# Optimization experiments

Hardware: AMD Instinct MI355X
Metric: run time of the kernel (lower is better)

Reference implementation:

```python
import jax, jax.numpy as jnp
import numpy as np

B, N, D, H = 32, 64, 128, 256
LN_EPS = 1e-5


def _mlp(x, W1, b1, g, beta, W2, b2):
    # Linear -> LayerNorm -> GELU (exact erf) -> Linear
    h = x @ W1 + b1
    mu = jnp.mean(h, axis=-1, keepdims=True)
    var = jnp.var(h, axis=-1, keepdims=True)
    h = (h - mu) * jax.lax.rsqrt(var + LN_EPS) * g + beta
    h = jax.nn.gelu(h, approximate=False)
    return h @ W2 + b2


def setup_inputs() -> dict:
    key = jax.random.key(0)
    ks = jax.random.split(key, 10)
    s = lambda fan_in: 1.0 / np.sqrt(fan_in)
    return {
        "slots": jax.random.normal(ks[0], (B, N, D), dtype=jnp.float32),
        "adjacency": jax.random.uniform(ks[1], (B, N, N), dtype=jnp.float32),
        # edge_net params
        "We1": jax.random.uniform(ks[2], (2 * D, H), minval=-s(2 * D), maxval=s(2 * D), dtype=jnp.float32),
        "be1": jnp.zeros((H,), jnp.float32),
        "ge": jnp.ones((H,), jnp.float32),
        "bge": jnp.zeros((H,), jnp.float32),
        "We2": jax.random.uniform(ks[3], (H, D), minval=-s(H), maxval=s(H), dtype=jnp.float32),
        "be2": jnp.zeros((D,), jnp.float32),
        # node_net params
        "Wn1": jax.random.uniform(ks[4], (2 * D, H), minval=-s(2 * D), maxval=s(2 * D), dtype=jnp.float32),
        "bn1": jnp.zeros((H,), jnp.float32),
        "gn": jnp.ones((H,), jnp.float32),
        "bgn": jnp.zeros((H,), jnp.float32),
        "Wn2": jax.random.uniform(ks[5], (H, D), minval=-s(H), maxval=s(H), dtype=jnp.float32),
        "bn2": jnp.zeros((D,), jnp.float32),
    }


def reference(slots, adjacency, We1, be1, ge, bge, We2, be2, Wn1, bn1, gn, bgn, Wn2, bn2):
    b, n, d = slots.shape
    # all-pairs edge features: receiver i, sender j -> [B,N,N,2D]
    ei = jnp.broadcast_to(slots[:, :, None, :], (b, n, n, d))
    ej = jnp.broadcast_to(slots[:, None, :, :], (b, n, n, d))
    edge_feat = jnp.concatenate([ei, ej], axis=-1)
    edge_out = _mlp(edge_feat, We1, be1, ge, bge, We2, be2)  # [B,N,N,D]
    # mask diagonal (i != j) and weight by adjacency, then reduce over j
    mask = 1.0 - jnp.eye(n, dtype=slots.dtype)
    w = adjacency * mask  # [B,N,N]
    messages = jnp.einsum('bij,bijd->bid', w, edge_out)
    node_input = jnp.concatenate([slots, messages], axis=-1)
    delta = _mlp(node_input, Wn1, bn1, gn, bgn, Wn2, bn2)
    return slots + delta
```

## Files before the change

### kernel.cpp

```cpp
#include <hip/hip_runtime.h>

#define NB 32
#define NN 64
#define ND 128
#define NH 256
#define LN_EPS 1e-5f
#define IBLK 4
#define RP 4

__device__ __forceinline__ float gelu_fast(float x) {
    const float z  = fabsf(x) * 0.70710678118654752440f;
    const float t  = __builtin_amdgcn_rcpf(fmaf(0.3275911f, z, 1.0f));
    float p = fmaf(1.061405429f, t, -1.453152027f);
    p = fmaf(p, t, 1.421413741f);
    p = fmaf(p, t, -0.284496736f);
    p = fmaf(p, t, 0.254829592f);
    p = p * t;
    const float e  = __expf(-z * z);
    const float er = copysignf(fmaf(-p, e, 1.0f), x);
    const float sx = 0.5f * x;
    return fmaf(sx, er, sx);
}

__global__ __launch_bounds__(256) void k_pq(const float* __restrict__ slots,
                                            const float* __restrict__ We1,
                                            const float* __restrict__ be1,
                                            float* __restrict__ Pt,
                                            float* __restrict__ Qm) {
    const int r0 = blockIdx.x * RP;
    const int t  = threadIdx.x;
    float pt[RP], qq[RP];
    const float bb = be1[t];
    #pragma unroll
    for (int r = 0; r < RP; ++r) { pt[r] = bb; qq[r] = 0.f; }
    const float* w1 = We1 + t;
    #pragma unroll 2
    for (int dc = 0; dc < ND / 4; ++dc) {
        float xs[RP][4];
        #pragma unroll
        for (int r = 0; r < RP; ++r) {
            const float4 x4 = ((const float4*)(slots + (size_t)(r0 + r) * ND))[dc];
            xs[r][0] = x4.x; xs[r][1] = x4.y; xs[r][2] = x4.z; xs[r][3] = x4.w;
        }
        #pragma unroll
        for (int i = 0; i < 4; ++i) {
            const int d = dc * 4 + i;
            const float wt  = w1[d * NH];
            const float wbt = w1[(ND + d) * NH];
            #pragma unroll
            for (int r = 0; r < RP; ++r) {
                pt[r] = fmaf(xs[r][i], wt,  pt[r]);
                qq[r] = fmaf(xs[r][i], wbt, qq[r]);
            }
        }
    }
    #pragma unroll
    for (int r = 0; r < RP; ++r) {
        Pt[(size_t)(r0 + r) * NH + t] = pt[r];
        Qm[(size_t)(r0 + r) * NH + t] = qq[r];
    }
}

__global__ __launch_bounds__(256) void k_fused(
    const float* __restrict__ slots,
    const float* __restrict__ adj,
    const float* __restrict__ Pt,
    const float* __restrict__ Qm,
    const float* __restrict__ ge,  const float* __restrict__ bge,
    const float* __restrict__ We2, const float* __restrict__ be2,
    const float* __restrict__ Wn1, const float* __restrict__ bn1,
    const float* __restrict__ gn,  const float* __restrict__ bgn,
    const float* __restrict__ Wn2, const float* __restrict__ bn2,
    float* __restrict__ out)
{
    __shared__ float  lds_pt[IBLK][NH];
    __shared__ float  lds_x [IBLK][ND];
    __shared__ float4 lds_wmr[IBLK][NN];
    __shared__ float  lds_s [4][IBLK][NH];
    __shared__ float  lds_sf[IBLK][NH];
    __shared__ float  lds_nin[IBLK][2 * ND];
    __shared__ float  lds_g [IBLK][NH];
    __shared__ float  lds_redA[4][IBLK], lds_redB[4][IBLK];
    __shared__ float  lds_wsum[IBLK];
    __shared__ float  lds_mu[IBLK], lds_rr[IBLK];

    const int blk  = blockIdx.x;
    const int b    = blk >> 4;
    const int i0   = (blk & 15) * IBLK;
    const int r0   = b * NN + i0;
    const int t    = threadIdx.x;
    const int lane = t & 63;
    const int wave = t >> 6;
    const int c    = t & 127;
    const int rg   = t >> 7;

    #pragma unroll
    for (int r = 0; r < IBLK; ++r)
        lds_pt[r][t] = Pt[(size_t)(r0 + r) * NH + t];
    lds_x[rg][c]     = slots[(size_t)(r0 + rg) * ND + c];
    lds_x[rg + 2][c] = slots[(size_t)(r0 + rg + 2) * ND + c];
    {
        float av = adj[(size_t)(r0 + wave) * NN + lane];
        if (lane == i0 + wave) av = 0.f;
        lds_wmr[wave][lane].x = av;
        float ws = av;
        #pragma unroll
        for (int off = 32; off; off >>= 1) ws += __shfl_xor(ws, off);
        if (lane == 0) lds_wsum[wave] = ws;
    }
    __syncthreads();

    {
        float a[IBLK], bq[IBLK];
        #pragma unroll
        for (int r = 0; r < IBLK; ++r) { const float p = lds_pt[r][t]; a[r] = p; bq[r] = p * p; }
        #pragma unroll
        for (int off = 32; off; off >>= 1) {
            #pragma unroll
            for (int r = 0; r < IBLK; ++r) {
                a[r]  += __shfl_xor(a[r],  off);
                bq[r] += __shfl_xor(bq[r], off);
            }
        }
        if (lane == 0) {
            #pragma unroll
            for (int r = 0; r < IBLK; ++r) { lds_redA[wave][r] = a[r]; lds_redB[wave][r] = bq[r]; }
        }
    }
    const int jp   = t >> 2;
    const int part = t & 3;
    float cd[IBLK] = {0.f, 0.f, 0.f, 0.f};
    float qs = 0.f, qs2 = 0.f;
    {
        const float4* qrow = (const float4*)(Qm + ((size_t)b * NN + jp) * NH) + part * 16;
        #pragma unroll 4
        for (int k = 0; k < 16; ++k) {
            const int kk = (k + part * 4) & 15;
            const float4 q = qrow[kk];
            qs  += (q.x + q.y) + (q.z + q.w);
            qs2  = fmaf(q.x, q.x, fmaf(q.y, q.y, fmaf(q.z, q.z, fmaf(q.w, q.w, qs2))));
            #pragma unroll
            for (int r = 0; r < IBLK; ++r) {
                const float4 p = ((const float4*)lds_pt[r])[part * 16 + kk];
                cd[r] = fmaf(p.x, q.x, fmaf(p.y, q.y, fmaf(p.z, q.z, fmaf(p.w, q.w, cd[r]))));
            }
        }
        #pragma unroll
        for (int off = 1; off < 4; off <<= 1) {
            qs += __shfl_xor(qs, off); qs2 += __shfl_xor(qs2, off);
            #pragma unroll
            for (int r = 0; r < IBLK; ++r) cd[r] += __shfl_xor(cd[r], off);
        }
    }
    __syncthreads();
    if (part == 0) {
        const float inv = 1.0f / NH;
        #pragma unroll
        for (int r = 0; r < IBLK; ++r) {
            const float SP1 = (lds_redA[0][r] + lds_redA[1][r]) + (lds_redA[2][r] + lds_redA[3][r]);
            const float SP2 = (lds_redB[0][r] + lds_redB[1][r]) + (lds_redB[2][r] + lds_redB[3][r]);
            const float mu  = (SP1 + qs) * inv;
            const float e2  = (SP2 + 2.f * cd[r] + qs2) * inv;
            lds_wmr[r][jp].y = mu;
            lds_wmr[r][jp].z = __builtin_amdgcn_rsqf(e2 - mu * mu + LN_EPS);
        }
    }
    __syncthreads();

    float4 P[IBLK], A[IBLK];
    #pragma unroll
    for (int r = 0; r < IBLK; ++r) {
        P[r] = ((const float4*)lds_pt[r])[lane];
        A[r] = make_float4(0.f, 0.f, 0.f, 0.f);
    }
    const float4 G  = ((const float4*)ge)[lane];
    const float4 Bg = ((const float4*)bge)[lane];
    const float4* Qb = (const float4*)(Qm + (size_t)b * NN * NH);
    #pragma unroll 2
    for (int jj = wave; jj < NN; jj += 4) {
        const float4 q = Qb[jj * (NH / 4) + lane];
        #pragma unroll
        for (int r = 0; r < IBLK; ++r) {
            const float4 wmr = lds_wmr[r][jj];
            const float wj = wmr.x, mu = wmr.y, rr = wmr.z;
            float h, u;
            h = P[r].x + q.x; u = fmaf((h - mu) * rr, G.x, Bg.x); A[r].x = fmaf(wj, gelu_fast(u), A[r].x);
            h = P[r].y + q.y; u = fmaf((h - mu) * rr, G.y, Bg.y); A[r].y = fmaf(wj, gelu_fast(u), A[r].y);
            h = P[r].z + q.z; u = fmaf((h - mu) * rr, G.z, Bg.z); A[r].z = fmaf(wj, gelu_fast(u), A[r].z);
            h = P[r].w + q.w; u = fmaf((h - mu) * rr, G.w, Bg.w); A[r].w = fmaf(wj, gelu_fast(u), A[r].w);
        }
    }
    #pragma unroll
    for (int r = 0; r < IBLK; ++r)
        ((float4*)&lds_s[wave][r][0])[lane] = A[r];
    __syncthreads();
    #pragma unroll
    for (int r = 0; r < IBLK; ++r)
        lds_sf[r][t] = (lds_s[0][r][t] + lds_s[1][r][t]) + (lds_s[2][r][t] + lds_s[3][r][t]);
    __syncthreads();

    {
        const int ra = rg, rb = rg + 2;
        float ma = lds_wsum[ra] * be2[c];
        float mb = lds_wsum[rb] * be2[c];
        const float* w2 = We2 + c;
        #pragma unroll 2
        for (int kc = 0; kc < NH / 4; ++kc) {
            const float4 sa = ((const float4*)lds_sf[ra])[kc];
            const float4 sb = ((const float4*)lds_sf[rb])[kc];
            const float w0 = w2[(4 * kc + 0) * ND];
            const float wA = w2[(4 * kc + 1) * ND];
            const float wB = w2[(4 * kc + 2) * ND];
            const float wC = w2[(4 * kc + 3) * ND];
            ma = fmaf(sa.x, w0, fmaf(sa.y, wA, fmaf(sa.z, wB, fmaf(sa.w, wC, ma))));
            mb = fmaf(sb.x, w0, fmaf(sb.y, wA, fmaf(sb.z, wB, fmaf(sb.w, wC, mb))));
        }
        lds_nin[ra][c] = lds_x[ra][c];  lds_nin[ra][ND + c] = ma;
        lds_nin[rb][c] = lds_x[rb][c];  lds_nin[rb][ND + c] = mb;
    }
    __syncthreads();

    float h[IBLK];
    {
        const float bb = bn1[t];
        #pragma unroll
        for (int r = 0; r < IBLK; ++r) h[r] = bb;
        const float* wn1 = Wn1 + t;
        #pragma unroll 2
        for (int kc = 0; kc < (2 * ND) / 4; ++kc) {
            float4 n4[IBLK];
            #pragma unroll
            for (int r = 0; r < IBLK; ++r) n4[r] = ((const float4*)lds_nin[r])[kc];
            const float w0 = wn1[(4 * kc + 0) * NH];
            const float wA = wn1[(4 * kc + 1) * NH];
            const float wB = wn1[(4 * kc + 2) * NH];
            const float wC = wn1[(4 * kc + 3) * NH];
            #pragma unroll
            for (int r = 0; r < IBLK; ++r)
                h[r] = fmaf(n4[r].x, w0, fmaf(n4[r].y, wA, fmaf(n4[r].z, wB, fmaf(n4[r].w, wC, h[r]))));
        }
    }
    {
        float a2[IBLK], b2[IBLK];
        #pragma unroll
        for (int r = 0; r < IBLK; ++r) { a2[r] = h[r]; b2[r] = h[r] * h[r]; }
        #pragma unroll
        for (int off = 32; off; off >>= 1) {
            #pragma unroll
            for (int r = 0; r < IBLK; ++r) {
                a2[r] += __shfl_xor(a2[r], off);
                b2[r] += __shfl_xor(b2[r], off);
            }
        }
        if (lane == 0) {
            #pragma unroll
            for (int r = 0; r < IBLK; ++r) { lds_redA[wave][r] = a2[r]; lds_redB[wave][r] = b2[r]; }
        }
    }
    __syncthreads();
    if (t < IBLK) {
        const float S1 = (lds_redA[0][t] + lds_redA[1][t]) + (lds_redA[2][t] + lds_redA[3][t]);
        const float S2 = (lds_redB[0][t] + lds_redB[1][t]) + (lds_redB[2][t] + lds_redB[3][t]);
        const float mu  = S1 * (1.0f / NH);
        const float var = S2 * (1.0f / NH) - mu * mu;
        lds_mu[t] = mu;
        lds_rr[t] = __builtin_amdgcn_rsqf(var + LN_EPS);
    }
    __syncthreads();
    {
        const float g = gn[t], bg = bgn[t];
        #pragma unroll
        for (int r = 0; r < IBLK; ++r)
            lds_g[r][t] = gelu_fast(fmaf((h[r] - lds_mu[r]) * lds_rr[r], g, bg));
    }
    __syncthreads();

    {
        const int ra = rg, rb = rg + 2;
        float da = bn2[c], db = bn2[c];
        const float* w2 = Wn2 + c;
        #pragma unroll 2
        for (int kc = 0; kc < NH / 4; ++kc) {
            const float4 ga = ((const float4*)lds_g[ra])[kc];
            const float4 gb = ((const float4*)lds_g[rb])[kc];
            const float w0 = w2[(4 * kc + 0) * ND];
            const float wA = w2[(4 * kc + 1) * ND];
            const float wB = w2[(4 * kc + 2) * ND];
            const float wC = w2[(4 * kc + 3) * ND];
            da = fmaf(ga.x, w0, fmaf(ga.y, wA, fmaf(ga.z, wB, fmaf(ga.w, wC, da))));
            db = fmaf(gb.x, w0, fmaf(gb.y, wA, fmaf(gb.z, wB, fmaf(gb.w, wC, db))));
        }
        out[(size_t)(r0 + ra) * ND + c] = lds_x[ra][c] + da;
        out[(size_t)(r0 + rb) * ND + c] = lds_x[rb][c] + db;
    }
}

extern "C" void kernel_launch(void* const* d_in, const int* in_sizes, int n_in,
                              void* d_out, int out_size, void* d_ws, size_t ws_size,
                              hipStream_t stream) {
    const float* slots = (const float*)d_in[0];
    const float* adj   = (const float*)d_in[1];
    const float* We1   = (const float*)d_in[2];
    const float* be1   = (const float*)d_in[3];
    const float* ge    = (const float*)d_in[4];
    const float* bge   = (const float*)d_in[5];
    const float* We2   = (const float*)d_in[6];
    const float* be2   = (const float*)d_in[7];
    const float* Wn1   = (const float*)d_in[8];
    const float* bn1   = (const float*)d_in[9];
    const float* gn    = (const float*)d_in[10];
    const float* bgn   = (const float*)d_in[11];
    const float* Wn2   = (const float*)d_in[12];
    const float* bn2   = (const float*)d_in[13];
    float* out = (float*)d_out;

    float* Ptw = (float*)d_ws;
    float* Qw  = Ptw + (size_t)NB * NN * NH;

    k_pq   <<<NB * NN / RP,   256, 0, stream>>>(slots, We1, be1, Ptw, Qw);
    k_fused<<<NB * NN / IBLK, 256, 0, stream>>>(slots, adj, Ptw, Qw, ge, bge, We2, be2,
                                                Wn1, bn1, gn, bgn, Wn2, bn2, out);
}
```

Before: 63.30 us.

## Fold We2 into Wn1 and split the fused kernel into message and node stages

Precomputes WC = We2·Wn1[D:] and v = be2·Wn1[D:] so the message projection and the first node linear merge into a single 256x256 matmul. The slots part of the node input (slots·Wn1[:D]) is computed alongside P and Q in the projection kernel. The old fused kernel is split into a message kernel with IBLK=2, giving twice as many blocks, and a node-MLP kernel that handles 8 rows per block. This trades extra launches, extra global round-trips and a per-call weight-fold kernel for more parallelism and better weight reuse in the node MLP.

```diff
diff --git a/kernel.cpp b/kernel.cpp
--- a/kernel.cpp
+++ b/kernel.cpp
@@ -5,8 +5,7 @@
 #define ND 128
 #define NH 256
 #define LN_EPS 1e-5f
-#define IBLK 4
-#define RP 4
+#define IBLK 2
 
 __device__ __forceinline__ float gelu_fast(float x) {
     const float z  = fabsf(x) * 0.70710678118654752440f;
@@ -22,91 +21,117 @@
     return fmaf(sx, er, sx);
 }
 
-__global__ __launch_bounds__(256) void k_pq(const float* __restrict__ slots,
+__global__ __launch_bounds__(256) void k_prep(const float* __restrict__ We2,
+                                              const float* __restrict__ be2,
+                                              const float* __restrict__ Wn1,
+                                              float* __restrict__ WC,
+                                              float* __restrict__ v) {
+    const int t = threadIdx.x;
+    if (blockIdx.x == 64) {
+        __shared__ float bs[ND];
+        if (t < ND) bs[t] = be2[t];
+        __syncthreads();
+        float acc = 0.f;
+        #pragma unroll 4
+        for (int d = 0; d < ND; ++d) acc = fmaf(bs[d], Wn1[(ND + d) * NH + t], acc);
+        v[t] = acc;
+        return;
+    }
+    const int k0 = blockIdx.x * 4;
+    __shared__ float ws[4][ND];
+    #pragma unroll
+    for (int i = 0; i < 2; ++i) {
+        const int idx = t + i * 256;
+        ws[idx >> 7][idx & 127] = We2[(k0 + (idx >> 7)) * ND + (idx & 127)];
+    }
+    __syncthreads();
+    float acc[4] = {0.f, 0.f, 0.f, 0.f};
+    #pragma unroll 4
+    for (int d = 0; d < ND; ++d) {
+        const float wn = Wn1[(ND + d) * NH + t];
+        #pragma unroll
+        for (int r = 0; r < 4; ++r) acc[r] = fmaf(ws[r][d], wn, acc[r]);
+    }
+    #pragma unroll
+    for (int r = 0; r < 4; ++r) WC[(k0 + r) * NH + t] = acc[r];
+}
+
+__global__ __launch_bounds__(512) void k_pq(const float* __restrict__ slots,
                                             const float* __restrict__ We1,
                                             const float* __restrict__ be1,
+                                            const float* __restrict__ Wn1,
                                             float* __restrict__ Pt,
-                                            float* __restrict__ Qm) {
-    const int r0 = blockIdx.x * RP;
-    const int t  = threadIdx.x;
-    float pt[RP], qq[RP];
-    const float bb = be1[t];
-    #pragma unroll
-    for (int r = 0; r < RP; ++r) { pt[r] = bb; qq[r] = 0.f; }
-    const float* w1 = We1 + t;
-    #pragma unroll 2
-    for (int dc = 0; dc < ND / 4; ++dc) {
-        float xs[RP][4];
-        #pragma unroll
-        for (int r = 0; r < RP; ++r) {
-            const float4 x4 = ((const float4*)(slots + (size_t)(r0 + r) * ND))[dc];
-            xs[r][0] = x4.x; xs[r][1] = x4.y; xs[r][2] = x4.z; xs[r][3] = x4.w;
-        }
-        #pragma unroll
-        for (int i = 0; i < 4; ++i) {
-            const int d = dc * 4 + i;
-            const float wt  = w1[d * NH];
-            const float wbt = w1[(ND + d) * NH];
-            #pragma unroll
-            for (int r = 0; r < RP; ++r) {
-                pt[r] = fmaf(xs[r][i], wt,  pt[r]);
-                qq[r] = fmaf(xs[r][i], wbt, qq[r]);
-            }
-        }
-    }
-    #pragma unroll
-    for (int r = 0; r < RP; ++r) {
-        Pt[(size_t)(r0 + r) * NH + t] = pt[r];
-        Qm[(size_t)(r0 + r) * NH + t] = qq[r];
-    }
-}
-
-__global__ __launch_bounds__(256) void k_fused(
-    const float* __restrict__ slots,
+                                            float* __restrict__ Qm,
+                                            float* __restrict__ XW) {
+    __shared__ float xs[8][ND];
+    const int r0   = blockIdx.x * 8;
+    const int t    = threadIdx.x;
+    const int c    = t & 255;
+    const int half = t >> 8;
+    #pragma unroll
+    for (int i = 0; i < 2; ++i) {
+        const int idx = t + i * 512;
+        xs[idx >> 7][idx & 127] = slots[(size_t)(r0 + (idx >> 7)) * ND + (idx & 127)];
+    }
+    __syncthreads();
+    float pt[4], qq[4], xw[4];
+    const float bb = be1[c];
+    #pragma unroll
+    for (int r = 0; r < 4; ++r) { pt[r] = bb; qq[r] = 0.f; xw[r] = 0.f; }
+    #pragma unroll 4
+    for (int d = 0; d < ND; ++d) {
+        const float wt  = We1[d * NH + c];
+        const float wbt = We1[(ND + d) * NH + c];
+        const float wn  = Wn1[d * NH + c];
+        #pragma unroll
+        for (int r = 0; r < 4; ++r) {
+            const float x = xs[half * 4 + r][d];
+            pt[r] = fmaf(x, wt,  pt[r]);
+            qq[r] = fmaf(x, wbt, qq[r]);
+            xw[r] = fmaf(x, wn,  xw[r]);
+        }
+    }
+    #pragma unroll
+    for (int r = 0; r < 4; ++r) {
+        const size_t row = (size_t)(r0 + half * 4 + r);
+        Pt[row * NH + c] = pt[r];
+        Qm[row * NH + c] = qq[r];
+        XW[row * NH + c] = xw[r];
+    }
+}
+
+__global__ __launch_bounds__(256) void k_msg(
     const float* __restrict__ adj,
     const float* __restrict__ Pt,
     const float* __restrict__ Qm,
     const float* __restrict__ ge,  const float* __restrict__ bge,
-    const float* __restrict__ We2, const float* __restrict__ be2,
-    const float* __restrict__ Wn1, const float* __restrict__ bn1,
-    const float* __restrict__ gn,  const float* __restrict__ bgn,
-    const float* __restrict__ Wn2, const float* __restrict__ bn2,
-    float* __restrict__ out)
+    float* __restrict__ Sw, float* __restrict__ wsumw)
 {
     __shared__ float  lds_pt[IBLK][NH];
-    __shared__ float  lds_x [IBLK][ND];
     __shared__ float4 lds_wmr[IBLK][NN];
-    __shared__ float  lds_s [4][IBLK][NH];
-    __shared__ float  lds_sf[IBLK][NH];
-    __shared__ float  lds_nin[IBLK][2 * ND];
-    __shared__ float  lds_g [IBLK][NH];
+    __shared__ float  lds_s[4][IBLK][NH];
     __shared__ float  lds_redA[4][IBLK], lds_redB[4][IBLK];
-    __shared__ float  lds_wsum[IBLK];
-    __shared__ float  lds_mu[IBLK], lds_rr[IBLK];
 
     const int blk  = blockIdx.x;
-    const int b    = blk >> 4;
-    const int i0   = (blk & 15) * IBLK;
+    const int b    = blk >> 5;
+    const int i0   = (blk & 31) * IBLK;
     const int r0   = b * NN + i0;
     const int t    = threadIdx.x;
     const int lane = t & 63;
     const int wave = t >> 6;
-    const int c    = t & 127;
-    const int rg   = t >> 7;
 
     #pragma unroll
     for (int r = 0; r < IBLK; ++r)
         lds_pt[r][t] = Pt[(size_t)(r0 + r) * NH + t];
-    lds_x[rg][c]     = slots[(size_t)(r0 + rg) * ND + c];
-    lds_x[rg + 2][c] = slots[(size_t)(r0 + rg + 2) * ND + c];
-    {
-        float av = adj[(size_t)(r0 + wave) * NN + lane];
-        if (lane == i0 + wave) av = 0.f;
-        lds_wmr[wave][lane].x = av;
-        float ws = av;
-        #pragma unroll
-        for (int off = 32; off; off >>= 1) ws += __shfl_xor(ws, off);
-        if (lane == 0) lds_wsum[wave] = ws;
+    if (t < IBLK * NN) {
+        const int r = t >> 6, l = t & 63;
+        float av = adj[(size_t)(r0 + r) * NN + l];
+        if (l == i0 + r) av = 0.f;
+        lds_wmr[r][l].x = av;
+        float wsv = av;
+        #pragma unroll
+        for (int off = 32; off; off >>= 1) wsv += __shfl_xor(wsv, off);
+        if (l == 0) wsumw[r0 + r] = wsv;
     }
     __syncthreads();
 
@@ -129,7 +154,7 @@
     }
     const int jp   = t >> 2;
     const int part = t & 3;
-    float cd[IBLK] = {0.f, 0.f, 0.f, 0.f};
+    float cd[IBLK] = {0.f, 0.f};
     float qs = 0.f, qs2 = 0.f;
     {
         const float4* qrow = (const float4*)(Qm + ((size_t)b * NN + jp) * NH) + part * 16;
@@ -176,7 +201,7 @@
     const float4 G  = ((const float4*)ge)[lane];
     const float4 Bg = ((const float4*)bge)[lane];
     const float4* Qb = (const float4*)(Qm + (size_t)b * NN * NH);
-    #pragma unroll 2
+    #pragma unroll 4
     for (int jj = wave; jj < NN; jj += 4) {
         const float4 q = Qb[jj * (NH / 4) + lane];
         #pragma unroll
@@ -196,71 +221,80 @@
     __syncthreads();
     #pragma unroll
     for (int r = 0; r < IBLK; ++r)
-        lds_sf[r][t] = (lds_s[0][r][t] + lds_s[1][r][t]) + (lds_s[2][r][t] + lds_s[3][r][t]);
-    __syncthreads();
-
-    {
-        const int ra = rg, rb = rg + 2;
-        float ma = lds_wsum[ra] * be2[c];
-        float mb = lds_wsum[rb] * be2[c];
-        const float* w2 = We2 + c;
-        #pragma unroll 2
-        for (int kc = 0; kc < NH / 4; ++kc) {
-            const float4 sa = ((const float4*)lds_sf[ra])[kc];
-            const float4 sb = ((const float4*)lds_sf[rb])[kc];
-            const float w0 = w2[(4 * kc + 0) * ND];
-            const float wA = w2[(4 * kc + 1) * ND];
-            const float wB = w2[(4 * kc + 2) * ND];
-            const float wC = w2[(4 * kc + 3) * ND];
-            ma = fmaf(sa.x, w0, fmaf(sa.y, wA, fmaf(sa.z, wB, fmaf(sa.w, wC, ma))));
-            mb = fmaf(sb.x, w0, fmaf(sb.y, wA, fmaf(sb.z, wB, fmaf(sb.w, wC, mb))));
-        }
-        lds_nin[ra][c] = lds_x[ra][c];  lds_nin[ra][ND + c] = ma;
-        lds_nin[rb][c] = lds_x[rb][c];  lds_nin[rb][ND + c] = mb;
-    }
-    __syncthreads();
-
-    float h[IBLK];
-    {
-        const float bb = bn1[t];
-        #pragma unroll
-        for (int r = 0; r < IBLK; ++r) h[r] = bb;
-        const float* wn1 = Wn1 + t;
-        #pragma unroll 2
-        for (int kc = 0; kc < (2 * ND) / 4; ++kc) {
-            float4 n4[IBLK];
-            #pragma unroll
-            for (int r = 0; r < IBLK; ++r) n4[r] = ((const float4*)lds_nin[r])[kc];
-            const float w0 = wn1[(4 * kc + 0) * NH];
-            const float wA = wn1[(4 * kc + 1) * NH];
-            const float wB = wn1[(4 * kc + 2) * NH];
-            const float wC = wn1[(4 * kc + 3) * NH];
-            #pragma unroll
-            for (int r = 0; r < IBLK; ++r)
-                h[r] = fmaf(n4[r].x, w0, fmaf(n4[r].y, wA, fmaf(n4[r].z, wB, fmaf(n4[r].w, wC, h[r]))));
-        }
-    }
-    {
-        float a2[IBLK], b2[IBLK];
-        #pragma unroll
-        for (int r = 0; r < IBLK; ++r) { a2[r] = h[r]; b2[r] = h[r] * h[r]; }
+        Sw[(size_t)(r0 + r) * NH + t] =
+            (lds_s[0][r][t] + lds_s[1][r][t]) + (lds_s[2][r][t] + lds_s[3][r][t]);
+}
+
+__global__ __launch_bounds__(512) void k_node(
+    const float* __restrict__ slots,
+    const float* __restrict__ Sw, const float* __restrict__ wsumw,
+    const float* __restrict__ XW,
+    const float* __restrict__ WC, const float* __restrict__ v,
+    const float* __restrict__ bn1,
+    const float* __restrict__ gn,  const float* __restrict__ bgn,
+    const float* __restrict__ Wn2, const float* __restrict__ bn2,
+    float* __restrict__ out)
+{
+    __shared__ float lds_S[8][NH];
+    __shared__ float lds_g[8][NH];
+    __shared__ float lds_redA[8][4], lds_redB[8][4];
+    __shared__ float lds_ws[8];
+    __shared__ float lds_mu[8], lds_rr[8];
+
+    const int r0   = blockIdx.x * 8;
+    const int t    = threadIdx.x;
+    const int c    = t & 255;
+    const int half = t >> 8;
+    const int wave = t >> 6;
+    const int lane = t & 63;
+
+    #pragma unroll
+    for (int rr = 0; rr < 4; ++rr) {
+        const int row = half * 4 + rr;
+        lds_S[row][c] = Sw[(size_t)(r0 + row) * NH + c];
+    }
+    if (t < 8) lds_ws[t] = wsumw[r0 + t];
+    __syncthreads();
+
+    float acc[4];
+    {
+        const float b1 = bn1[c], vc = v[c];
+        #pragma unroll
+        for (int rr = 0; rr < 4; ++rr) {
+            const int row = half * 4 + rr;
+            acc[rr] = fmaf(lds_ws[row], vc, b1) + XW[(size_t)(r0 + row) * NH + c];
+        }
+    }
+    #pragma unroll 8
+    for (int k = 0; k < NH; ++k) {
+        const float w = WC[k * NH + c];
+        #pragma unroll
+        for (int rr = 0; rr < 4; ++rr) acc[rr] = fmaf(lds_S[half * 4 + rr][k], w, acc[rr]);
+    }
+
+    {
+        float a[4], bq[4];
+        #pragma unroll
+        for (int rr = 0; rr < 4; ++rr) { a[rr] = acc[rr]; bq[rr] = acc[rr] * acc[rr]; }
         #pragma unroll
         for (int off = 32; off; off >>= 1) {
             #pragma unroll
-            for (int r = 0; r < IBLK; ++r) {
-                a2[r] += __shfl_xor(a2[r], off);
-                b2[r] += __shfl_xor(b2[r], off);
+            for (int rr = 0; rr < 4; ++rr) {
+                a[rr]  += __shfl_xor(a[rr],  off);
+                bq[rr] += __shfl_xor(bq[rr], off);
             }
         }
         if (lane == 0) {
             #pragma unroll
-            for (int r = 0; r < IBLK; ++r) { lds_redA[wave][r] = a2[r]; lds_redB[wave][r] = b2[r]; }
-        }
-    }
-    __syncthreads();
-    if (t < IBLK) {
-        const float S1 = (lds_redA[0][t] + lds_redA[1][t]) + (lds_redA[2][t] + lds_redA[3][t]);
-        const float S2 = (lds_redB[0][t] + lds_redB[1][t]) + (lds_redB[2][t] + lds_redB[3][t]);
+            for (int rr = 0; rr < 4; ++rr) { lds_redA[wave][rr] = a[rr]; lds_redB[wave][rr] = bq[rr]; }
+        }
+    }
+    __syncthreads();
+    if (t < 8) {
+        const int h = t >> 2, rr = t & 3;
+        float S1 = 0.f, S2 = 0.f;
+        #pragma unroll
+        for (int w_ = 0; w_ < 4; ++w_) { S1 += lds_redA[h * 4 + w_][rr]; S2 += lds_redB[h * 4 + w_][rr]; }
         const float mu  = S1 * (1.0f / NH);
         const float var = S2 * (1.0f / NH) - mu * mu;
         lds_mu[t] = mu;
@@ -268,30 +302,27 @@
     }
     __syncthreads();
     {
-        const float g = gn[t], bg = bgn[t];
-        #pragma unroll
-        for (int r = 0; r < IBLK; ++r)
-            lds_g[r][t] = gelu_fast(fmaf((h[r] - lds_mu[r]) * lds_rr[r], g, bg));
-    }
-    __syncthreads();
-
-    {
-        const int ra = rg, rb = rg + 2;
-        float da = bn2[c], db = bn2[c];
-        const float* w2 = Wn2 + c;
-        #pragma unroll 2
-        for (int kc = 0; kc < NH / 4; ++kc) {
-            const float4 ga = ((const float4*)lds_g[ra])[kc];
-            const float4 gb = ((const float4*)lds_g[rb])[kc];
-            const float w0 = w2[(4 * kc + 0) * ND];
-            const float wA = w2[(4 * kc + 1) * ND];
-            const float wB = w2[(4 * kc + 2) * ND];
-            const float wC = w2[(4 * kc + 3) * ND];
-            da = fmaf(ga.x, w0, fmaf(ga.y, wA, fmaf(ga.z, wB, fmaf(ga.w, wC, da))));
-            db = fmaf(gb.x, w0, fmaf(gb.y, wA, fmaf(gb.z, wB, fmaf(gb.w, wC, db))));
-        }
-        out[(size_t)(r0 + ra) * ND + c] = lds_x[ra][c] + da;
-        out[(size_t)(r0 + rb) * ND + c] = lds_x[rb][c] + db;
+        const float g = gn[c], bg = bgn[c];
+        #pragma unroll
+        for (int rr = 0; rr < 4; ++rr) {
+            const int row = half * 4 + rr;
+            lds_g[row][c] = gelu_fast(fmaf((acc[rr] - lds_mu[row]) * lds_rr[row], g, bg));
+        }
+    }
+    __syncthreads();
+
+    {
+        const int c2 = t & 127, grp = t >> 7;
+        const int ra = grp * 2, rb = grp * 2 + 1;
+        float d0 = bn2[c2], d1 = d0;
+        #pragma unroll 8
+        for (int k = 0; k < NH; ++k) {
+            const float w = Wn2[k * ND + c2];
+            d0 = fmaf(lds_g[ra][k], w, d0);
+            d1 = fmaf(lds_g[rb][k], w, d1);
+        }
+        out[(size_t)(r0 + ra) * ND + c2] = slots[(size_t)(r0 + ra) * ND + c2] + d0;
+        out[(size_t)(r0 + rb) * ND + c2] = slots[(size_t)(r0 + rb) * ND + c2] + d1;
     }
 }
 
@@ -314,10 +345,18 @@
     const float* bn2   = (const float*)d_in[13];
     float* out = (float*)d_out;
 
-    float* Ptw = (float*)d_ws;
-    float* Qw  = Ptw + (size_t)NB * NN * NH;
-
-    k_pq   <<<NB * NN / RP,   256, 0, stream>>>(slots, We1, be1, Ptw, Qw);
-    k_fused<<<NB * NN / IBLK, 256, 0, stream>>>(slots, adj, Ptw, Qw, ge, bge, We2, be2,
-                                                Wn1, bn1, gn, bgn, Wn2, bn2, out);
-}
+    const size_t RN = (size_t)NB * NN;
+    float* Ptw   = (float*)d_ws;
+    float* Qw    = Ptw   + RN * NH;
+    float* XWw   = Qw    + RN * NH;
+    float* Sww   = XWw   + RN * NH;
+    float* wsumw = Sww   + RN * NH;
+    float* WCw   = wsumw + RN;
+    float* vw    = WCw   + (size_t)NH * NH;
+
+    k_prep<<<65,            256, 0, stream>>>(We2, be2, Wn1, WCw, vw);
+    k_pq  <<<(int)(RN / 8), 512, 0, stream>>>(slots, We1, be1, Wn1, Ptw, Qw, XWw);
+    k_msg <<<(int)(RN / IBLK), 256, 0, stream>>>(adj, Ptw, Qw, ge, bge, Sww, wsumw);
+    k_node<<<(int)(RN / 8), 512, 0, stream>>>(slots, Sww, wsumw, XWw, WCw, vw,
+                                              bn1, gn, bgn, Wn2, bn2, out);
+}
```

Result: slower. 83.97 us (+32.6%).
